# Kernel optimization log

Hardware: AMD Instinct MI355X
Metric: run time of the kernel (lower is better)

## Reference

```python
import jax, jax.numpy as jnp
import numpy as np

N_NODES = 50000
N_EDGES = 800000
D_FEAT = 100


def setup_inputs() -> dict:
    key = jax.random.key(0)
    ks = jax.random.split(key, 10)
    s = 0.1
    x = jax.random.normal(ks[0], (N_NODES, D_FEAT), dtype=jnp.float32)
    edge_index = jax.random.randint(ks[1], (2, N_EDGES), 0, N_NODES, dtype=jnp.int32)
    return {
        "x": x,
        "edge_index": edge_index,
        "convW0": jax.random.normal(ks[2], (100, 100), jnp.float32) * s,
        "convb0": jnp.zeros((100,), jnp.float32),
        "convW1": jax.random.normal(ks[3], (100, 100), jnp.float32) * s,
        "convb1": jnp.zeros((100,), jnp.float32),
        "linW0": jax.random.normal(ks[4], (100, 10), jnp.float32) * s,
        "linb0": jnp.zeros((10,), jnp.float32),
        "linW1": jax.random.normal(ks[5], (10, 1), jnp.float32) * s,
        "linb1": jnp.zeros((1,), jnp.float32),
    }


def _gcn_conv(x, W, b, src, dst, n):
    """PyG GCNConv: h = x @ W; out[i] = sum_{(j->i)} d_j^{-1/2} d_i^{-1/2} h[j] + b,
    with self-loops already included in (src, dst)."""
    h = x @ W  # [N, out]
    deg = jax.ops.segment_sum(jnp.ones(src.shape[0], x.dtype), dst, num_segments=n)
    dinv = jnp.where(deg > 0, jax.lax.rsqrt(deg), jnp.zeros_like(deg))
    norm = dinv[src] * dinv[dst]  # [E_tot]
    msg = norm[:, None] * h[src]  # gather [E_tot, out]
    out = jax.ops.segment_sum(msg, dst, num_segments=n)  # scatter-add
    return out + b


def reference(x, edge_index, convW0, convb0, convW1, convb1, linW0, linb0, linW1, linb1):
    n = x.shape[0]
    # global-norm division (x.div(torch.norm(x).detach()))
    nm = jax.lax.stop_gradient(jnp.linalg.norm(x))
    x = x / nm
    # NOTE: original re-assigns x via sklearn SelectKBest(chi2, k=100) on raw data.x;
    # that is non-differentiable data preprocessing, so we assume x already holds the
    # k=100 selected features.
    loops = jnp.arange(n, dtype=edge_index.dtype)
    src = jnp.concatenate([edge_index[0], loops])  # self-loops appended
    dst = jnp.concatenate([edge_index[1], loops])
    x = _gcn_conv(x, convW0, convb0, src, dst, n)
    x = _gcn_conv(x, convW1, convb1, src, dst, n)
    # MLP head: ReLU between layers, no activation after the last (loop breaks)
    x = jax.nn.relu(x @ linW0 + linb0)
    x = x @ linW1 + linb1
    return x.T  # [1, N]
```

## Files before the change

kernel.cpp:

```cpp
#include <hip/hip_runtime.h>

#define NN 50000
#define DF 100
#define NE 800000
#define ELLW 64

__device__ __forceinline__ float wredf(float v) {
    #pragma unroll
    for (int o = 32; o > 0; o >>= 1) v += __shfl_down(v, o, 64);
    return v;
}

__global__ __launch_bounds__(256) void k_sumsq(const float* __restrict__ x,
                                               float* __restrict__ acc) {
    const float4* x4 = (const float4*)x;
    const int n4 = NN * DF / 4;
    float s = 0.f;
    for (int i = blockIdx.x * 256 + threadIdx.x; i < n4; i += gridDim.x * 256) {
        float4 v = x4[i];
        s += v.x * v.x + v.y * v.y + v.z * v.z + v.w * v.w;
    }
    s = wredf(s);
    __shared__ float p[4];
    int lane = threadIdx.x & 63, w = threadIdx.x >> 6;
    if (lane == 0) p[w] = s;
    __syncthreads();
    if (threadIdx.x == 0) atomicAdd(acc, p[0] + p[1] + p[2] + p[3]);
}

__global__ __launch_bounds__(256) void k_fill(const int* __restrict__ src,
                                              const int* __restrict__ dst,
                                              int* __restrict__ cursor,
                                              int* __restrict__ ell) {
    int e = blockIdx.x * 256 + threadIdx.x;
    if (e >= NE) return;
    int d = dst[e];
    int p = atomicAdd(&cursor[d], 1);
    if (p < ELLW) ell[d * ELLW + p] = src[e];
}

__global__ __launch_bounds__(256) void k_wprep(const float* __restrict__ W0,
                                               const float* __restrict__ W1,
                                               const float* __restrict__ cb0,
                                               const float* __restrict__ cb1,
                                               const float* __restrict__ L0,
                                               const float* __restrict__ lb0,
                                               const float* __restrict__ sumsq,
                                               float* __restrict__ Wz,
                                               float* __restrict__ u,
                                               float* __restrict__ cvec) {
    __shared__ float WA[1000];
    int t = threadIdx.x;
    for (int o = t; o < 1000; o += 256) {
        int j = o / 10, m = o % 10;
        float s = 0.f;
        for (int k = 0; k < 100; ++k) s += W1[j * 100 + k] * L0[k * 10 + m];
        WA[o] = s;
    }
    __syncthreads();
    float sc = rsqrtf(*sumsq);
    for (int o = t; o < 1000; o += 256) {
        int i = o / 10, m = o % 10;
        float s = 0.f;
        for (int k = 0; k < 100; ++k) s += W0[i * 100 + k] * WA[k * 10 + m];
        Wz[o] = sc * s;
    }
    if (t < 10) {
        float su = 0.f, scv = 0.f;
        for (int k = 0; k < 100; ++k) {
            su  += cb0[k] * WA[k * 10 + t];
            scv += cb1[k] * L0[k * 10 + t];
        }
        u[t] = su;
        cvec[t] = scv + lb0[t];
    }
}

__global__ __launch_bounds__(256) void k_ygemm(const float* __restrict__ x,
                                               const float* __restrict__ Wz,
                                               const int* __restrict__ cursor,
                                               float* __restrict__ gp) {
    __shared__ float w[1000];
    for (int o = threadIdx.x; o < 1000; o += 256) w[o] = Wz[o];
    __syncthreads();
    int i = blockIdx.x * 256 + threadIdx.x;
    if (i >= NN) return;
    const float4* r4 = (const float4*)(x + i * 100);
    float h[10];
    #pragma unroll
    for (int m = 0; m < 10; ++m) h[m] = 0.f;
    for (int kk = 0; kk < 25; ++kk) {
        float4 a = r4[kk];
        #pragma unroll
        for (int j = 0; j < 4; ++j) {
            float av = ((const float*)&a)[j];
            int k = kk * 4 + j;
            #pragma unroll
            for (int m = 0; m < 10; ++m) h[m] += av * w[k * 10 + m];
        }
    }
    float d = rsqrtf((float)(cursor[i] + 1));
    float o16[16];
    #pragma unroll
    for (int m = 0; m < 10; ++m) o16[m] = d * h[m];
    o16[10] = d;
    o16[11] = o16[12] = o16[13] = o16[14] = o16[15] = 0.f;
    float4* dst4 = (float4*)(gp + i * 16);
    #pragma unroll
    for (int q = 0; q < 4; ++q) dst4[q] = *(float4*)&o16[q * 4];
}

__global__ __launch_bounds__(256) void k_agg1(const float* __restrict__ gp,
                                              const int* __restrict__ cursor,
                                              const int* __restrict__ ell,
                                              float* __restrict__ tb) {
    int n = (blockIdx.x * 256 + threadIdx.x) >> 6;
    int l = threadIdx.x & 63;
    int g = l >> 4, lane16 = l & 15;
    int cnt = min(cursor[n], ELLW);
    const int* row = ell + n * ELLW;
    float acc = (g == 0) ? gp[n * 16 + lane16] : 0.f;
    int k = g;
    for (; k + 4 < cnt; k += 8) {
        int s0 = row[k], s1 = row[k + 4];
        acc += gp[s0 * 16 + lane16];
        acc += gp[s1 * 16 + lane16];
    }
    if (k < cnt) acc += gp[row[k] * 16 + lane16];
    acc += __shfl_xor(acc, 16, 64);
    acc += __shfl_xor(acc, 32, 64);
    if (l < 16) {
        float dv = rsqrtf((float)(cnt + 1));
        float o = (lane16 < 10) ? dv * dv * acc : (lane16 == 10 ? dv * acc : 0.f);
        tb[n * 16 + lane16] = o;
    }
}

__global__ __launch_bounds__(256) void k_agg2(const float* __restrict__ tb,
                                              const int* __restrict__ cursor,
                                              const int* __restrict__ ell,
                                              const float* __restrict__ u,
                                              const float* __restrict__ cvec,
                                              const float* __restrict__ L1,
                                              const float* __restrict__ lb1,
                                              float* __restrict__ out) {
    __shared__ float su[10], sc[10], sl[10];
    if (threadIdx.x < 10) {
        su[threadIdx.x] = u[threadIdx.x];
        sc[threadIdx.x] = cvec[threadIdx.x];
        sl[threadIdx.x] = L1[threadIdx.x];
    }
    __syncthreads();
    int n = (blockIdx.x * 256 + threadIdx.x) >> 6;
    int l = threadIdx.x & 63;
    int g = l >> 4, lane16 = l & 15;
    int cnt = min(cursor[n], ELLW);
    const int* row = ell + n * ELLW;
    float acc = (g == 0) ? tb[n * 16 + lane16] : 0.f;
    int k = g;
    for (; k + 4 < cnt; k += 8) {
        int s0 = row[k], s1 = row[k + 4];
        acc += tb[s0 * 16 + lane16];
        acc += tb[s1 * 16 + lane16];
    }
    if (k < cnt) acc += tb[row[k] * 16 + lane16];
    acc += __shfl_xor(acc, 16, 64);
    acc += __shfl_xor(acc, 32, 64);
    if (l < 16) {
        float dv = rsqrtf((float)(cnt + 1));
        float v = tb[n * 16 + 10];
        float hidden = 0.f;
        if (lane16 < 10)
            hidden = fmaxf(dv * acc + v * su[lane16] + sc[lane16], 0.f) * sl[lane16];
        #pragma unroll
        for (int o = 8; o; o >>= 1) hidden += __shfl_down(hidden, o, 16);
        if (lane16 == 0) out[n] = hidden + lb1[0];
    }
}

extern "C" void kernel_launch(void* const* d_in, const int* in_sizes, int n_in,
                              void* d_out, int out_size, void* d_ws, size_t ws_size,
                              hipStream_t stream) {
    const float* x   = (const float*)d_in[0];
    const int*   ei  = (const int*)d_in[1];
    const int*   src = ei;
    const int*   dst = ei + NE;
    const float* W0  = (const float*)d_in[2];
    const float* cb0 = (const float*)d_in[3];
    const float* W1  = (const float*)d_in[4];
    const float* cb1 = (const float*)d_in[5];
    const float* lw0 = (const float*)d_in[6];
    const float* lb0 = (const float*)d_in[7];
    const float* lw1 = (const float*)d_in[8];
    const float* lb1 = (const float*)d_in[9];
    float* out = (float*)d_out;

    char* ws = (char*)d_ws;
    float* acc     = (float*)(ws + 0);
    int*   cursor  = (int*)  (ws + 256);
    const size_t zspan = 200256;
    float* Wz      = (float*)(ws + 200320);
    float* uvec    = (float*)(ws + 204416);
    float* cvec    = (float*)(ws + 204544);
    int*   ell     = (int*)  (ws + 204800);
    float* gp      = (float*)(ws + 13004800);
    float* tb      = (float*)(ws + 16204800);

    hipMemsetAsync(d_ws, 0, zspan, stream);
    k_sumsq <<<1024, 256, 0, stream>>>(x, acc);
    k_fill  <<<(NE + 255) / 256, 256, 0, stream>>>(src, dst, cursor, ell);
    k_wprep <<<1, 256, 0, stream>>>(W0, W1, cb0, cb1, lw0, lb0, acc, Wz, uvec, cvec);
    k_ygemm <<<(NN + 255) / 256, 256, 0, stream>>>(x, Wz, cursor, gp);
    k_agg1  <<<NN * 64 / 256, 256, 0, stream>>>(gp, cursor, ell, tb);
    k_agg2  <<<NN * 64 / 256, 256, 0, stream>>>(tb, cursor, ell, uvec, cvec, lw1, lb1, out);
}
```

Measured before the change: 221.4 us.

## Fuse preprocessing kernels and shard ELL build per XCC with compacted rows

Merges the sum-of-squares, ELL fill and weight-prep kernels into one launch, using block-index ranges to pick the role. Edge insertion uses per-XCC cursors with workgroup-scope atomics and 16-slot sub-buckets per XCC, and k_ygemm then compacts them into a padded row with a sentinel zero node. The global-norm scale moves from Wz into agg1 so weight prep no longer waits on the reduction. The aggregation loops are unrolled four-wide with independent accumulators. The cost is larger workspace memsets and a serial compaction loop per node. Workgroup-scope atomics on a global counter shared by all blocks on one XCC rely on hardware coherence behaviour, and each XCC bucket holds at most 16 edges per node.

```diff
diff --git a/kernel.cpp b/kernel.cpp
--- a/kernel.cpp
+++ b/kernel.cpp
@@ -3,7 +3,12 @@
 #define NN 50000
 #define DF 100
 #define NE 800000
-#define ELLW 64
+
+__device__ __forceinline__ int xcc_id() {
+    int x;
+    asm volatile("s_getreg_b32 %0, hwreg(HW_REG_XCC_ID)" : "=s"(x));
+    return x & 7;
+}
 
 __device__ __forceinline__ float wredf(float v) {
     #pragma unroll
@@ -11,80 +16,105 @@
     return v;
 }
 
-__global__ __launch_bounds__(256) void k_sumsq(const float* __restrict__ x,
-                                               float* __restrict__ acc) {
-    const float4* x4 = (const float4*)x;
-    const int n4 = NN * DF / 4;
-    float s = 0.f;
-    for (int i = blockIdx.x * 256 + threadIdx.x; i < n4; i += gridDim.x * 256) {
-        float4 v = x4[i];
-        s += v.x * v.x + v.y * v.y + v.z * v.z + v.w * v.w;
-    }
-    s = wredf(s);
-    __shared__ float p[4];
-    int lane = threadIdx.x & 63, w = threadIdx.x >> 6;
-    if (lane == 0) p[w] = s;
-    __syncthreads();
-    if (threadIdx.x == 0) atomicAdd(acc, p[0] + p[1] + p[2] + p[3]);
-}
-
-__global__ __launch_bounds__(256) void k_fill(const int* __restrict__ src,
-                                              const int* __restrict__ dst,
-                                              int* __restrict__ cursor,
-                                              int* __restrict__ ell) {
-    int e = blockIdx.x * 256 + threadIdx.x;
-    if (e >= NE) return;
-    int d = dst[e];
-    int p = atomicAdd(&cursor[d], 1);
-    if (p < ELLW) ell[d * ELLW + p] = src[e];
-}
-
-__global__ __launch_bounds__(256) void k_wprep(const float* __restrict__ W0,
-                                               const float* __restrict__ W1,
-                                               const float* __restrict__ cb0,
-                                               const float* __restrict__ cb1,
-                                               const float* __restrict__ L0,
-                                               const float* __restrict__ lb0,
-                                               const float* __restrict__ sumsq,
-                                               float* __restrict__ Wz,
-                                               float* __restrict__ u,
-                                               float* __restrict__ cvec) {
-    __shared__ float WA[1000];
-    int t = threadIdx.x;
-    for (int o = t; o < 1000; o += 256) {
-        int j = o / 10, m = o % 10;
+__global__ __launch_bounds__(256) void k_pre(const float* __restrict__ x,
+                                             float* __restrict__ acc,
+                                             const int* __restrict__ src,
+                                             const int* __restrict__ dst,
+                                             int* __restrict__ cur,
+                                             int* __restrict__ ell,
+                                             const float* __restrict__ W0,
+                                             const float* __restrict__ W1,
+                                             const float* __restrict__ cb0,
+                                             const float* __restrict__ cb1,
+                                             const float* __restrict__ L0,
+                                             const float* __restrict__ lb0,
+                                             float* __restrict__ Wz,
+                                             float* __restrict__ uvec,
+                                             float* __restrict__ cvec) {
+    int b = blockIdx.x, t = threadIdx.x;
+    if (b < 3125) {
+        int e = b * 256 + t;
+        int d = dst[e];
+        int g = xcc_id();
+        int p = __hip_atomic_fetch_add(&cur[g * NN + d], 1, __ATOMIC_RELAXED,
+                                       __HIP_MEMORY_SCOPE_WORKGROUP);
+        if (p < 16) ell[d * 128 + g * 16 + p] = src[e];
+    } else if (b < 4149) {
+        const float4* x4 = (const float4*)x;
+        const int n4 = NN * DF / 4;
+        int tid = (b - 3125) * 256 + t, stride = 1024 * 256;
         float s = 0.f;
-        for (int k = 0; k < 100; ++k) s += W1[j * 100 + k] * L0[k * 10 + m];
-        WA[o] = s;
-    }
-    __syncthreads();
-    float sc = rsqrtf(*sumsq);
-    for (int o = t; o < 1000; o += 256) {
-        int i = o / 10, m = o % 10;
-        float s = 0.f;
-        for (int k = 0; k < 100; ++k) s += W0[i * 100 + k] * WA[k * 10 + m];
-        Wz[o] = sc * s;
-    }
-    if (t < 10) {
-        float su = 0.f, scv = 0.f;
-        for (int k = 0; k < 100; ++k) {
-            su  += cb0[k] * WA[k * 10 + t];
-            scv += cb1[k] * L0[k * 10 + t];
-        }
-        u[t] = su;
-        cvec[t] = scv + lb0[t];
+        for (int i = tid; i < n4; i += stride) {
+            float4 v = x4[i];
+            s += v.x * v.x + v.y * v.y + v.z * v.z + v.w * v.w;
+        }
+        s = wredf(s);
+        __shared__ float p[4];
+        int lane = t & 63, w = t >> 6;
+        if (lane == 0) p[w] = s;
+        __syncthreads();
+        if (t == 0) atomicAdd(acc, p[0] + p[1] + p[2] + p[3]);
+    } else {
+        __shared__ float WA[1000];
+        for (int o = t; o < 1000; o += 256) {
+            int j = o / 10, m = o % 10;
+            float s = 0.f;
+            for (int k = 0; k < 100; ++k) s += W1[j * 100 + k] * L0[k * 10 + m];
+            WA[o] = s;
+        }
+        __syncthreads();
+        for (int o = t; o < 1000; o += 256) {
+            int i = o / 10, m = o % 10;
+            float s = 0.f;
+            for (int k = 0; k < 100; ++k) s += W0[i * 100 + k] * WA[k * 10 + m];
+            Wz[o] = s;
+        }
+        if (t < 10) {
+            float su = 0.f, scv = 0.f;
+            for (int k = 0; k < 100; ++k) {
+                su  += cb0[k] * WA[k * 10 + t];
+                scv += cb1[k] * L0[k * 10 + t];
+            }
+            uvec[t] = su;
+            cvec[t] = scv + lb0[t];
+        }
     }
 }
 
 __global__ __launch_bounds__(256) void k_ygemm(const float* __restrict__ x,
                                                const float* __restrict__ Wz,
-                                               const int* __restrict__ cursor,
+                                               const int* __restrict__ cur,
+                                               int* __restrict__ ell,
+                                               int* __restrict__ cnt4A,
+                                               float* __restrict__ dinvA,
                                                float* __restrict__ gp) {
     __shared__ float w[1000];
     for (int o = threadIdx.x; o < 1000; o += 256) w[o] = Wz[o];
     __syncthreads();
     int i = blockIdx.x * 256 + threadIdx.x;
-    if (i >= NN) return;
+    if (i > NN) return;
+    if (i == NN) {
+        float4 z = {0.f, 0.f, 0.f, 0.f};
+        float4* d4 = (float4*)(gp + NN * 16);
+        d4[0] = z; d4[1] = z; d4[2] = z; d4[3] = z;
+        return;
+    }
+    int* rp = ell + i * 128;
+    int c0 = min(cur[i], 16);
+    int total = c0;
+    int wpos = c0;
+    for (int r = 1; r < 8; ++r) {
+        int cr = min(cur[r * NN + i], 16);
+        total += cr;
+        for (int j = 0; j < cr; ++j) rp[wpos + j] = rp[r * 16 + j];
+        wpos += cr;
+    }
+    int cnt4 = (total + 3) & ~3;
+    for (int j = total; j < cnt4; ++j) rp[j] = NN;
+    cnt4A[i] = cnt4;
+    float dv = rsqrtf((float)(total + 1));
+    dinvA[i] = dv;
+
     const float4* r4 = (const float4*)(x + i * 100);
     float h[10];
     #pragma unroll
@@ -99,11 +129,10 @@
             for (int m = 0; m < 10; ++m) h[m] += av * w[k * 10 + m];
         }
     }
-    float d = rsqrtf((float)(cursor[i] + 1));
     float o16[16];
     #pragma unroll
-    for (int m = 0; m < 10; ++m) o16[m] = d * h[m];
-    o16[10] = d;
+    for (int m = 0; m < 10; ++m) o16[m] = dv * h[m];
+    o16[10] = dv;
     o16[11] = o16[12] = o16[13] = o16[14] = o16[15] = 0.f;
     float4* dst4 = (float4*)(gp + i * 16);
     #pragma unroll
@@ -111,67 +140,85 @@
 }
 
 __global__ __launch_bounds__(256) void k_agg1(const float* __restrict__ gp,
-                                              const int* __restrict__ cursor,
+                                              const int* __restrict__ cnt4A,
+                                              const float* __restrict__ dinvA,
                                               const int* __restrict__ ell,
+                                              const float* __restrict__ sumsq,
                                               float* __restrict__ tb) {
     int n = (blockIdx.x * 256 + threadIdx.x) >> 6;
     int l = threadIdx.x & 63;
     int g = l >> 4, lane16 = l & 15;
-    int cnt = min(cursor[n], ELLW);
-    const int* row = ell + n * ELLW;
-    float acc = (g == 0) ? gp[n * 16 + lane16] : 0.f;
-    int k = g;
-    for (; k + 4 < cnt; k += 8) {
-        int s0 = row[k], s1 = row[k + 4];
-        acc += gp[s0 * 16 + lane16];
-        acc += gp[s1 * 16 + lane16];
-    }
-    if (k < cnt) acc += gp[row[k] * 16 + lane16];
+    if (n > NN) return;
+    if (n == NN) {
+        if (l < 16) tb[NN * 16 + lane16] = 0.f;
+        return;
+    }
+    int cnt4 = cnt4A[n];
+    const int* rp = ell + n * 128;
+    float a0 = (g == 0) ? gp[n * 16 + lane16] : 0.f;
+    float a1 = 0.f, a2 = 0.f, a3 = 0.f;
+    int J = cnt4 >> 2, k = g;
+    for (; J >= 4; J -= 4, k += 16) {
+        int i0 = rp[k], i1 = rp[k + 4], i2 = rp[k + 8], i3 = rp[k + 12];
+        a0 += gp[i0 * 16 + lane16];
+        a1 += gp[i1 * 16 + lane16];
+        a2 += gp[i2 * 16 + lane16];
+        a3 += gp[i3 * 16 + lane16];
+    }
+    for (; J > 0; --J, k += 4) a0 += gp[rp[k] * 16 + lane16];
+    float acc = (a0 + a1) + (a2 + a3);
     acc += __shfl_xor(acc, 16, 64);
     acc += __shfl_xor(acc, 32, 64);
     if (l < 16) {
-        float dv = rsqrtf((float)(cnt + 1));
-        float o = (lane16 < 10) ? dv * dv * acc : (lane16 == 10 ? dv * acc : 0.f);
+        float dv = dinvA[n];
+        float sc = rsqrtf(*sumsq);
+        float o = (lane16 < 10) ? sc * dv * dv * acc
+                                : (lane16 == 10 ? dv * acc : 0.f);
         tb[n * 16 + lane16] = o;
     }
 }
 
 __global__ __launch_bounds__(256) void k_agg2(const float* __restrict__ tb,
-                                              const int* __restrict__ cursor,
+                                              const int* __restrict__ cnt4A,
+                                              const float* __restrict__ dinvA,
                                               const int* __restrict__ ell,
                                               const float* __restrict__ u,
                                               const float* __restrict__ cvec,
                                               const float* __restrict__ L1,
                                               const float* __restrict__ lb1,
                                               float* __restrict__ out) {
-    __shared__ float su[10], sc[10], sl[10];
+    __shared__ float su[10], scv[10], sl[10];
     if (threadIdx.x < 10) {
         su[threadIdx.x] = u[threadIdx.x];
-        sc[threadIdx.x] = cvec[threadIdx.x];
+        scv[threadIdx.x] = cvec[threadIdx.x];
         sl[threadIdx.x] = L1[threadIdx.x];
     }
     __syncthreads();
     int n = (blockIdx.x * 256 + threadIdx.x) >> 6;
     int l = threadIdx.x & 63;
     int g = l >> 4, lane16 = l & 15;
-    int cnt = min(cursor[n], ELLW);
-    const int* row = ell + n * ELLW;
-    float acc = (g == 0) ? tb[n * 16 + lane16] : 0.f;
-    int k = g;
-    for (; k + 4 < cnt; k += 8) {
-        int s0 = row[k], s1 = row[k + 4];
-        acc += tb[s0 * 16 + lane16];
-        acc += tb[s1 * 16 + lane16];
-    }
-    if (k < cnt) acc += tb[row[k] * 16 + lane16];
+    int cnt4 = cnt4A[n];
+    const int* rp = ell + n * 128;
+    float a0 = (g == 0) ? tb[n * 16 + lane16] : 0.f;
+    float a1 = 0.f, a2 = 0.f, a3 = 0.f;
+    int J = cnt4 >> 2, k = g;
+    for (; J >= 4; J -= 4, k += 16) {
+        int i0 = rp[k], i1 = rp[k + 4], i2 = rp[k + 8], i3 = rp[k + 12];
+        a0 += tb[i0 * 16 + lane16];
+        a1 += tb[i1 * 16 + lane16];
+        a2 += tb[i2 * 16 + lane16];
+        a3 += tb[i3 * 16 + lane16];
+    }
+    for (; J > 0; --J, k += 4) a0 += tb[rp[k] * 16 + lane16];
+    float acc = (a0 + a1) + (a2 + a3);
     acc += __shfl_xor(acc, 16, 64);
     acc += __shfl_xor(acc, 32, 64);
     if (l < 16) {
-        float dv = rsqrtf((float)(cnt + 1));
+        float dv = dinvA[n];
         float v = tb[n * 16 + 10];
         float hidden = 0.f;
         if (lane16 < 10)
-            hidden = fmaxf(dv * acc + v * su[lane16] + sc[lane16], 0.f) * sl[lane16];
+            hidden = fmaxf(dv * acc + v * su[lane16] + scv[lane16], 0.f) * sl[lane16];
         #pragma unroll
         for (int o = 8; o; o >>= 1) hidden += __shfl_down(hidden, o, 16);
         if (lane16 == 0) out[n] = hidden + lb1[0];
@@ -197,20 +244,21 @@
 
     char* ws = (char*)d_ws;
     float* acc     = (float*)(ws + 0);
-    int*   cursor  = (int*)  (ws + 256);
-    const size_t zspan = 200256;
-    float* Wz      = (float*)(ws + 200320);
-    float* uvec    = (float*)(ws + 204416);
-    float* cvec    = (float*)(ws + 204544);
-    int*   ell     = (int*)  (ws + 204800);
-    float* gp      = (float*)(ws + 13004800);
-    float* tb      = (float*)(ws + 16204800);
+    int*   cur     = (int*)  (ws + 256);
+    const size_t zspan = 1600256;
+    float* Wz      = (float*)(ws + 1600512);
+    float* uvec    = (float*)(ws + 1604608);
+    float* cvec    = (float*)(ws + 1604736);
+    int*   ell     = (int*)  (ws + 1604864);
+    float* gp      = (float*)(ws + 27204864);
+    float* tb      = (float*)(ws + 30404992);
+    float* dinvA   = (float*)(ws + 33605120);
+    int*   cnt4A   = (int*)  (ws + 33805312);
 
     hipMemsetAsync(d_ws, 0, zspan, stream);
-    k_sumsq <<<1024, 256, 0, stream>>>(x, acc);
-    k_fill  <<<(NE + 255) / 256, 256, 0, stream>>>(src, dst, cursor, ell);
-    k_wprep <<<1, 256, 0, stream>>>(W0, W1, cb0, cb1, lw0, lb0, acc, Wz, uvec, cvec);
-    k_ygemm <<<(NN + 255) / 256, 256, 0, stream>>>(x, Wz, cursor, gp);
-    k_agg1  <<<NN * 64 / 256, 256, 0, stream>>>(gp, cursor, ell, tb);
-    k_agg2  <<<NN * 64 / 256, 256, 0, stream>>>(tb, cursor, ell, uvec, cvec, lw1, lb1, out);
-}
+    k_pre   <<<4150, 256, 0, stream>>>(x, acc, src, dst, cur, ell,
+                                       W0, W1, cb0, cb1, lw0, lb0, Wz, uvec, cvec);
+    k_ygemm <<<196, 256, 0, stream>>>(x, Wz, cur, ell, cnt4A, dinvA, gp);
+    k_agg1  <<<12501, 256, 0, stream>>>(gp, cnt4A, dinvA, ell, acc, tb);
+    k_agg2  <<<12500, 256, 0, stream>>>(tb, cnt4A, dinvA, ell, uvec, cvec, lw1, lb1, out);
+}
```

After: 211.1 us. 1.05x faster.
